# Optimization experiments

Measured on AMD Instinct MI355X. Metric: run time of the kernel, lower is better.

The kernel has to match this reference:

```python
import jax, jax.numpy as jnp
import numpy as np

N = 50000      # nodes
E = 800000     # edges (avg degree 16)
F_IN = 128     # input_dim
HID = 64       # hidden_dim
HEADS = 4      # heads on first layer only
G = 512        # number of graphs in batch
EPS = 1e-5
NEG_SLOPE = 0.2

# (in_dim, out_dim, heads) per GATv2 layer
LAYER_DIMS = [(F_IN, HID, HEADS), (HID * HEADS, HID, 1), (HID, HID, 1)]


def setup_inputs() -> dict:
    key = jax.random.key(0)
    ks = jax.random.split(key, 16)
    def rn(k, shape, fan_in):
        return jax.random.normal(k, shape, jnp.float32) / np.float32(np.sqrt(fan_in))
    inp = {}
    inp["x"] = jax.random.normal(ks[0], (N, F_IN), jnp.float32)
    inp["edge_index"] = jax.random.randint(ks[1], (2, E), 0, N)
    inp["batch"] = jnp.sort(jax.random.randint(ks[2], (N,), 0, G))
    i = 3
    for l, (din, dout, h) in enumerate(LAYER_DIMS):
        kk = jax.random.split(ks[i], 3)
        inp[f"Wl{l}"] = rn(kk[0], (din, h * dout), din)
        inp[f"bl{l}"] = jnp.zeros((h * dout,), jnp.float32)
        inp[f"Wr{l}"] = rn(kk[1], (din, h * dout), din)
        inp[f"br{l}"] = jnp.zeros((h * dout,), jnp.float32)
        inp[f"att{l}"] = rn(kk[2], (h, dout), dout)
        inp[f"bias{l}"] = jnp.zeros((h * dout,), jnp.float32)
        inp[f"ln_g{l}"] = jnp.ones((h * dout,), jnp.float32)
        inp[f"ln_b{l}"] = jnp.zeros((h * dout,), jnp.float32)
        i += 1
    inp["Wh1"] = rn(ks[i], (HID, HID), HID)
    inp["bh1"] = jnp.zeros((HID,), jnp.float32)
    inp["Wh2"] = rn(ks[i + 1], (HID, 1), HID)
    inp["bh2"] = jnp.zeros((1,), jnp.float32)
    return inp


def gatv2_layer(x, src, dst, Wl, bl, Wr, br, att, bias, heads, out_c):
    """PyG GATv2Conv (concat=True, share_weights=False, eval mode)."""
    n = x.shape[0]
    xl = (x @ Wl + bl).reshape(n, heads, out_c)   # messages (source side)
    xr = (x @ Wr + br).reshape(n, heads, out_c)   # destination side
    e = jax.nn.leaky_relu(xl[src] + xr[dst], NEG_SLOPE)          # [E,H,C]
    logit = jnp.einsum('ehc,hc->eh', e, att)                      # [E,H]
    m = jax.ops.segment_max(logit, dst, num_segments=n)           # segment-softmax
    ex = jnp.exp(logit - m[dst])
    den = jax.ops.segment_sum(ex, dst, num_segments=n)
    alpha = ex / den[dst]                                         # [E,H]
    out = jax.ops.segment_sum(alpha[:, :, None] * xl[src], dst, num_segments=n)
    return out.reshape(n, heads * out_c) + bias


def graph_layernorm(h, g, b):
    """PyG LayerNorm(mode='graph') with batch=None: normalize over all elements."""
    mu = h.mean()
    xc = h - mu
    var = (xc * xc).mean()
    return xc * jax.lax.rsqrt(var + EPS) * g + b


def reference(x, edge_index, batch,
              Wl0, bl0, Wr0, br0, att0, bias0, ln_g0, ln_b0,
              Wl1, bl1, Wr1, br1, att1, bias1, ln_g1, ln_b1,
              Wl2, bl2, Wr2, br2, att2, bias2, ln_g2, ln_b2,
              Wh1, bh1, Wh2, bh2):
    src, dst = edge_index[0], edge_index[1]
    layers = [
        (Wl0, bl0, Wr0, br0, att0, bias0, ln_g0, ln_b0),
        (Wl1, bl1, Wr1, br1, att1, bias1, ln_g1, ln_b1),
        (Wl2, bl2, Wr2, br2, att2, bias2, ln_g2, ln_b2),
    ]
    h = x
    for (Wl, bl, Wr, br, att, bias, g, b), (_, dout, heads) in zip(layers, LAYER_DIMS):
        h_in = h
        h = gatv2_layer(h, src, dst, Wl, bl, Wr, br, att, bias, heads, dout)
        h = graph_layernorm(h, g, b)
        h = jax.nn.relu(h)
        if h_in.shape[1] == h.shape[1]:   # residual only when widths match
            h = h + h_in
        # dropout: identity in eval mode
    # global mean pool over graphs
    counts = jax.ops.segment_sum(jnp.ones((h.shape[0], 1), h.dtype), batch, num_segments=G)
    Z = jax.ops.segment_sum(h, batch, num_segments=G) / jnp.maximum(counts, 1.0)
    logits = jax.nn.relu(Z @ Wh1 + bh1) @ Wh2 + bh2
    return logits
```

## Files before the change

### kernel.cpp

```cpp
#include <hip/hip_runtime.h>
#include <math.h>

#define NN 50000
#define NE 800000
#define NG 512
#define LRELU 0.2f
#define LN_EPS 1e-5
#define GCAP 128
#define NBUCK 256

typedef __attribute__((ext_vector_type(8))) short short8;
typedef __attribute__((ext_vector_type(4))) float f32x4;

__global__ void hist_kernel(const int* __restrict__ dst, int* __restrict__ deg) {
    int e = blockIdx.x * blockDim.x + threadIdx.x;
    if (e < NE) atomicAdd(&deg[dst[e]], 1);
}

__global__ __launch_bounds__(1024) void scan1(const int* __restrict__ deg,
                                              int* __restrict__ excl,
                                              int* __restrict__ bsum, int n) {
    __shared__ int s[1024];
    int tid = threadIdx.x;
    int gid = blockIdx.x * 1024 + tid;
    int v = (gid < n) ? deg[gid] : 0;
    s[tid] = v;
    __syncthreads();
    for (int off = 1; off < 1024; off <<= 1) {
        int t = (tid >= off) ? s[tid - off] : 0;
        __syncthreads();
        s[tid] += t;
        __syncthreads();
    }
    if (gid < n) excl[gid] = s[tid] - v;
    if (tid == 1023) bsum[blockIdx.x] = s[1023];
}

__global__ __launch_bounds__(1024) void scan3(int* __restrict__ row_ptr,
                                              int* __restrict__ cursor,
                                              const int* __restrict__ bsum, int n) {
    __shared__ int sbase;
    int tid = threadIdx.x;
    if (tid < 64) {
        int v = (tid < (int)blockIdx.x) ? bsum[tid] : 0;
        #pragma unroll
        for (int off = 32; off > 0; off >>= 1) v += __shfl_xor(v, off, 64);
        if (tid == 0) sbase = v;
    }
    __syncthreads();
    int gid = blockIdx.x * 1024 + tid;
    if (gid < n) {
        int v = row_ptr[gid] + sbase;
        row_ptr[gid] = v;
        cursor[gid] = v;
    }
    if (gid == 0) row_ptr[n] = NE;
}

__global__ void scatter_kernel(const int* __restrict__ src, const int* __restrict__ dst,
                               int* __restrict__ cursor, int* __restrict__ col_src) {
    int e = blockIdx.x * blockDim.x + threadIdx.x;
    if (e < NE) {
        int pos = atomicAdd(&cursor[dst[e]], 1);
        col_src[pos] = src[e];
    }
}

__device__ inline void split_bf16(float v, ushort& h, ushort& l) {
    unsigned ub = __float_as_uint(v);
    unsigned hh = (ub + 0x7FFFu + ((ub >> 16) & 1u)) >> 16;
    float vh = __uint_as_float(hh << 16);
    float r = v - vh;
    unsigned ur = __float_as_uint(r);
    unsigned ll = (ur + 0x7FFFu + ((ur >> 16) & 1u)) >> 16;
    h = (ushort)hh; l = (ushort)ll;
}

__global__ __launch_bounds__(256) void prep_w(const float* __restrict__ Wl0,
                                              const float* __restrict__ Wr0,
                                              const float* __restrict__ Wl1,
                                              const float* __restrict__ Wr1,
                                              const float* __restrict__ Wl2,
                                              const float* __restrict__ Wr2,
                                              ushort* __restrict__ wt) {
    int id = blockIdx.x * 256 + threadIdx.x;
    const float* W; int K, N, rel; ushort* hi;
    if (id < 65536) {
        W = (id < 32768) ? Wl0 : Wr0;
        rel = id & 32767; K = 128; N = 256;
        hi = wt + ((id < 32768) ? 0 : 65536);
    } else if (id < 98304) {
        int t = id - 65536;
        W = (t < 16384) ? Wl1 : Wr1;
        rel = t & 16383; K = 256; N = 64;
        hi = wt + 131072 + ((t < 16384) ? 0 : 32768);
    } else if (id < 106496) {
        int t = id - 98304;
        W = (t < 4096) ? Wl2 : Wr2;
        rel = t & 4095; K = 64; N = 64;
        hi = wt + 196608 + ((t < 4096) ? 0 : 8192);
    } else return;
    ushort* lo = hi + K * N;
    int n = rel / K, k = rel - n * K;
    ushort h, l;
    split_bf16(W[k * N + n], h, l);
    hi[rel] = h;
    lo[rel] = l;
}

template<int NCB, bool DOLN>
__global__ __launch_bounds__(256) void gemm_mfma(const float* __restrict__ A,
                                                 const ushort* __restrict__ Bh0,
                                                 const ushort* __restrict__ Bl0,
                                                 const float* __restrict__ bias0,
                                                 float* __restrict__ C0,
                                                 const ushort* __restrict__ Bh1,
                                                 const ushort* __restrict__ Bl1,
                                                 const float* __restrict__ bias1,
                                                 float* __restrict__ C1,
                                                 int M, int Ncol, int K,
                                                 const double* __restrict__ red,
                                                 int Mdiv,
                                                 const float* __restrict__ lng,
                                                 const float* __restrict__ lnb) {
    __shared__ ushort sAh[64][40];
    __shared__ ushort sAl[64][40];
    __shared__ ushort sBh[64 * NCB][40];
    __shared__ ushort sBl[64 * NCB][40];
    __shared__ float sstat[2];
    const ushort* Bhi = blockIdx.y ? Bh1 : Bh0;
    const ushort* Blo = blockIdx.y ? Bl1 : Bl0;
    const float*  bias = blockIdx.y ? bias1 : bias0;
    float*        C = blockIdx.y ? C1 : C0;
    const int tid = threadIdx.x;
    const int row0 = blockIdx.x * 64;
    const int w = tid >> 6, lane = tid & 63;
    const int fm = lane & 15;
    const int fk = (lane >> 4) * 8;
    float mu = 0.f, rstd = 0.f;
    if constexpr (DOLN) {
        if (tid < 64) {
            double sa = 0, sb = 0;
            for (int i = lane; i < NBUCK; i += 64) { sa += red[2 * i]; sb += red[2 * i + 1]; }
            #pragma unroll
            for (int off = 32; off > 0; off >>= 1) {
                sa += __shfl_xor(sa, off, 64);
                sb += __shfl_xor(sb, off, 64);
            }
            if (lane == 0) {
                double m_ = sa / Mdiv;
                double v_ = sb / Mdiv - m_ * m_;
                sstat[0] = (float)m_;
                sstat[1] = (float)(1.0 / sqrt(v_ + LN_EPS));
            }
        }
        __syncthreads();
        mu = sstat[0]; rstd = sstat[1];
    }
    f32x4 acc[4 * NCB] = {};

    for (int k0 = 0; k0 < K; k0 += 32) {
        __syncthreads();
        int f = tid;
        #pragma unroll
        for (int it = 0; it < 2; it++, f += 256) {
            int r = f >> 3, kc = (f & 7) * 4;
            int grow = row0 + r;
            float4 v = (grow < M) ? *(const float4*)&A[(size_t)grow * K + k0 + kc]
                                  : make_float4(0.f, 0.f, 0.f, 0.f);
            if constexpr (DOLN) {
                int c0 = k0 + kc;
                v.x = fmaxf((v.x - mu) * rstd * lng[c0 + 0] + lnb[c0 + 0], 0.f);
                v.y = fmaxf((v.y - mu) * rstd * lng[c0 + 1] + lnb[c0 + 1], 0.f);
                v.z = fmaxf((v.z - mu) * rstd * lng[c0 + 2] + lnb[c0 + 2], 0.f);
                v.w = fmaxf((v.w - mu) * rstd * lng[c0 + 3] + lnb[c0 + 3], 0.f);
            }
            ushort4 h, l;
            split_bf16(v.x, h.x, l.x);
            split_bf16(v.y, h.y, l.y);
            split_bf16(v.z, h.z, l.z);
            split_bf16(v.w, h.w, l.w);
            *(ushort4*)&sAh[r][kc] = h;
            *(ushort4*)&sAl[r][kc] = l;
        }
        int u = tid;
        #pragma unroll
        for (int it = 0; it < 2 * NCB; it++, u += 256) {
            int n = u >> 3, kc = (u & 7) * 4;
            *(ushort4*)&sBh[n][kc] = *(const ushort4*)&Bhi[(size_t)n * K + k0 + kc];
            *(ushort4*)&sBl[n][kc] = *(const ushort4*)&Blo[(size_t)n * K + k0 + kc];
        }
        __syncthreads();
        short8 ah = *(const short8*)&sAh[w * 16 + fm][fk];
        short8 al = *(const short8*)&sAl[w * 16 + fm][fk];
        #pragma unroll
        for (int c = 0; c < 4 * NCB; c++) {
            short8 bh = *(const short8*)&sBh[c * 16 + fm][fk];
            short8 bl = *(const short8*)&sBl[c * 16 + fm][fk];
            acc[c] = __builtin_amdgcn_mfma_f32_16x16x32_bf16(ah, bh, acc[c], 0, 0, 0);
            acc[c] = __builtin_amdgcn_mfma_f32_16x16x32_bf16(al, bh, acc[c], 0, 0, 0);
            acc[c] = __builtin_amdgcn_mfma_f32_16x16x32_bf16(ah, bl, acc[c], 0, 0, 0);
        }
    }
    const int orow = w * 16 + (lane >> 4) * 4;
    #pragma unroll
    for (int c = 0; c < 4 * NCB; c++) {
        int col = c * 16 + fm;
        float bv = bias[col];
        #pragma unroll
        for (int r = 0; r < 4; r++) {
            int grow = row0 + orow + r;
            if (grow < M) C[(size_t)grow * Ncol + col] = acc[c][r] + bv;
        }
    }
}

__device__ inline float dpp_red_add16(float x) {
    x += __int_as_float(__builtin_amdgcn_update_dpp(0, __float_as_int(x), 0xB1, 0xF, 0xF, true));
    x += __int_as_float(__builtin_amdgcn_update_dpp(0, __float_as_int(x), 0x4E, 0xF, 0xF, true));
    x += __int_as_float(__builtin_amdgcn_update_dpp(0, __float_as_int(x), 0x141, 0xF, 0xF, true));
    x += __int_as_float(__builtin_amdgcn_update_dpp(0, __float_as_int(x), 0x140, 0xF, 0xF, true));
    return x;
}

__device__ inline void gat_upd_fast(const float4& xv, const float4& rxr, const float4& ratt,
                                    float& m, float& sum, float4& acc) {
    float vx = xv.x + rxr.x; vx = fmaxf(vx, vx * LRELU);
    float vy = xv.y + rxr.y; vy = fmaxf(vy, vy * LRELU);
    float vz = xv.z + rxr.z; vz = fmaxf(vz, vz * LRELU);
    float vw = xv.w + rxr.w; vw = fmaxf(vw, vw * LRELU);
    float p = vx * ratt.x;
    p = fmaf(vy, ratt.y, p);
    p = fmaf(vz, ratt.z, p);
    p = fmaf(vw, ratt.w, p);
    p = dpp_red_add16(p);
    if (__all(p <= m)) {
        float e = __expf(p - m);
        sum += e;
        acc.x = fmaf(e, xv.x, acc.x);
        acc.y = fmaf(e, xv.y, acc.y);
        acc.z = fmaf(e, xv.z, acc.z);
        acc.w = fmaf(e, xv.w, acc.w);
    } else {
        float mn = fmaxf(m, p);
        float sc = __expf(m - mn);
        float e  = __expf(p - mn);
        sum = fmaf(sum, sc, e);
        acc.x = fmaf(acc.x, sc, e * xv.x);
        acc.y = fmaf(acc.y, sc, e * xv.y);
        acc.z = fmaf(acc.z, sc, e * xv.z);
        acc.w = fmaf(acc.w, sc, e * xv.w);
        m = mn;
    }
}

__global__ __launch_bounds__(256) void gat4(const float* __restrict__ xl,
                                            const float* __restrict__ xr,
                                            const float* __restrict__ att,
                                            const float* __restrict__ bias,
                                            const int* __restrict__ row_ptr,
                                            const int* __restrict__ col_src,
                                            float* __restrict__ out,
                                            double* __restrict__ red) {
    __shared__ int scol[4][GCAP + 8];
    __shared__ double bs1[4], bs2[4];
    const int tid = threadIdx.x;
    const int w = tid >> 6, lane = tid & 63;
    const int n = blockIdx.x * 4 + w;
    const int base = row_ptr[n];
    int deg = row_ptr[n + 1] - base;
    if (deg > GCAP) deg = GCAP;
    for (int j = lane; j < deg; j += 64) scol[w][j] = col_src[base + j];
    if (deg > 0 && lane < 8) scol[w][deg + lane] = col_src[base + deg - 1];
    const float4 rxr  = ((const float4*)(xr + (size_t)n * 256))[lane];
    const float4 ratt = ((const float4*)att)[lane];
    __syncthreads();

    float m = -1e30f, sum = 0.f;
    float4 acc = {0.f, 0.f, 0.f, 0.f};
    if (deg > 0) {
        auto LD = [&](int j) {
            return ((const float4*)(xl + (size_t)scol[w][j] * 256))[lane];
        };
        float4 b0 = LD(0), b1 = LD(1), b2 = LD(2), b3 = LD(3);
        int j = 0;
        for (; j + 4 <= deg; j += 4) {
            gat_upd_fast(b0, rxr, ratt, m, sum, acc); b0 = LD(j + 4);
            gat_upd_fast(b1, rxr, ratt, m, sum, acc); b1 = LD(j + 5);
            gat_upd_fast(b2, rxr, ratt, m, sum, acc); b2 = LD(j + 6);
            gat_upd_fast(b3, rxr, ratt, m, sum, acc); b3 = LD(j + 7);
        }
        int r = deg - j;
        if (r > 0) gat_upd_fast(b0, rxr, ratt, m, sum, acc);
        if (r > 1) gat_upd_fast(b1, rxr, ratt, m, sum, acc);
        if (r > 2) gat_upd_fast(b2, rxr, ratt, m, sum, acc);
    }
    float rden = (sum > 0.f) ? 1.f / sum : 0.f;
    float4 bv = ((const float4*)bias)[lane];
    float4 o;
    o.x = fmaf(acc.x, rden, bv.x);
    o.y = fmaf(acc.y, rden, bv.y);
    o.z = fmaf(acc.z, rden, bv.z);
    o.w = fmaf(acc.w, rden, bv.w);
    ((float4*)(out + (size_t)n * 256))[lane] = o;

    float z1 = o.x + o.y + o.z + o.w;
    float z2 = o.x * o.x + o.y * o.y + o.z * o.z + o.w * o.w;
    #pragma unroll
    for (int off = 32; off > 0; off >>= 1) {
        z1 += __shfl_xor(z1, off, 64);
        z2 += __shfl_xor(z2, off, 64);
    }
    if (lane == 0) { bs1[w] = (double)z1; bs2[w] = (double)z2; }
    __syncthreads();
    if (tid == 0) {
        double t1 = bs1[0] + bs1[1] + bs1[2] + bs1[3];
        double t2 = bs2[0] + bs2[1] + bs2[2] + bs2[3];
        int b = (blockIdx.x & (NBUCK - 1)) * 2;
        atomicAdd(&red[b], t1);
        atomicAdd(&red[b + 1], t2);
    }
}

__global__ __launch_bounds__(256) void gat1(const float* __restrict__ xl,
                                            const float* __restrict__ xr,
                                            const float* __restrict__ att,
                                            const float* __restrict__ bias,
                                            const int* __restrict__ row_ptr,
                                            const int* __restrict__ col_src,
                                            float* __restrict__ out,
                                            double* __restrict__ red) {
    __shared__ int scol[4][GCAP + 16];
    __shared__ double bs1[4], bs2[4];
    const int tid = threadIdx.x;
    const int w = tid >> 6, lane = tid & 63;
    const int n = blockIdx.x * 4 + w;
    const int g = lane >> 4, li = lane & 15;
    const int base = row_ptr[n];
    int deg = row_ptr[n + 1] - base;
    if (deg > GCAP) deg = GCAP;
    for (int j = lane; j < deg; j += 64) scol[w][j] = col_src[base + j];
    if (deg > 0 && lane < 16) scol[w][deg + lane] = col_src[base + deg - 1];
    const float4 rxr  = ((const float4*)(xr + (size_t)n * 64))[li];
    const float4 ratt = ((const float4*)att)[li];
    __syncthreads();

    float m = -1e30f, sum = 0.f;
    float4 acc = {0.f, 0.f, 0.f, 0.f};
    if (deg > 0) {
        auto LD = [&](int j) {
            return ((const float4*)(xl + (size_t)scol[w][j] * 64))[li];
        };
        float4 a = LD(g), b = LD(g + 4);
        for (int j = g; j < deg; j += 8) {
            gat_upd_fast(a, rxr, ratt, m, sum, acc); a = LD(j + 8);
            if (j + 4 < deg) { gat_upd_fast(b, rxr, ratt, m, sum, acc); b = LD(j + 12); }
        }
    }
    #pragma unroll
    for (int off = 16; off < 64; off <<= 1) {
        float m2 = __shfl_xor(m, off, 64);
        float z2 = __shfl_xor(sum, off, 64);
        float ax = __shfl_xor(acc.x, off, 64);
        float ay = __shfl_xor(acc.y, off, 64);
        float az = __shfl_xor(acc.z, off, 64);
        float aw = __shfl_xor(acc.w, off, 64);
        float M = fmaxf(m, m2);
        float e1 = __expf(m - M), e2 = __expf(m2 - M);
        sum   = sum   * e1 + z2 * e2;
        acc.x = acc.x * e1 + ax * e2;
        acc.y = acc.y * e1 + ay * e2;
        acc.z = acc.z * e1 + az * e2;
        acc.w = acc.w * e1 + aw * e2;
        m = M;
    }
    float rden = (sum > 0.f) ? 1.f / sum : 0.f;
    float4 bv = ((const float4*)bias)[li];
    float4 o;
    o.x = fmaf(acc.x, rden, bv.x);
    o.y = fmaf(acc.y, rden, bv.y);
    o.z = fmaf(acc.z, rden, bv.z);
    o.w = fmaf(acc.w, rden, bv.w);
    if (g == 0) ((float4*)(out + (size_t)n * 64))[li] = o;

    float z1 = (g == 0) ? (o.x + o.y + o.z + o.w) : 0.f;
    float z2 = (g == 0) ? (o.x * o.x + o.y * o.y + o.z * o.z + o.w * o.w) : 0.f;
    #pragma unroll
    for (int off = 32; off > 0; off >>= 1) {
        z1 += __shfl_xor(z1, off, 64);
        z2 += __shfl_xor(z2, off, 64);
    }
    if (lane == 0) { bs1[w] = (double)z1; bs2[w] = (double)z2; }
    __syncthreads();
    if (tid == 0) {
        double t1 = bs1[0] + bs1[1] + bs1[2] + bs1[3];
        double t2 = bs2[0] + bs2[1] + bs2[2] + bs2[3];
        int b = (blockIdx.x & (NBUCK - 1)) * 2;
        atomicAdd(&red[b], t1);
        atomicAdd(&red[b + 1], t2);
    }
}

#define PLB 256
__global__ __launch_bounds__(256) void pool_ln(const float* __restrict__ C2,
                                               const float* __restrict__ D,
                                               const double* __restrict__ red,
                                               const float* __restrict__ g1,
                                               const float* __restrict__ b1,
                                               const float* __restrict__ g2,
                                               const float* __restrict__ b2,
                                               const int* __restrict__ batch,
                                               float* __restrict__ Zsum,
                                               int* __restrict__ gcount) {
    __shared__ float sst[4];
    const int w = threadIdx.x >> 6;
    const int lane = threadIdx.x & 63;
    if (w < 2) {
        const double* rp = red + (w + 1) * 2 * NBUCK;
        double sa = 0, sb = 0;
        for (int i = lane; i < NBUCK; i += 64) { sa += rp[2 * i]; sb += rp[2 * i + 1]; }
        #pragma unroll
        for (int off = 32; off > 0; off >>= 1) {
            sa += __shfl_xor(sa, off, 64);
            sb += __shfl_xor(sb, off, 64);
        }
        if (lane == 0) {
            double m_ = sa / (double)(NN * 64);
            double v_ = sb / (double)(NN * 64) - m_ * m_;
            sst[w * 2]     = (float)m_;
            sst[w * 2 + 1] = (float)(1.0 / sqrt(v_ + LN_EPS));
        }
    }
    __syncthreads();
    const float mu1 = sst[0], r1 = sst[1], mu2 = sst[2], r2 = sst[3];
    const int wid = blockIdx.x * 4 + w;
    const int NW = PLB * 4;
    const int per = (NN + NW - 1) / NW;
    int n0 = wid * per;
    int n1 = n0 + per; if (n1 > NN) n1 = NN;
    if (n0 >= n1) return;
    const float ga = r1 * g1[lane], ba = fmaf(-mu1, ga, b1[lane]);
    const float gb = r2 * g2[lane], bb = fmaf(-mu2, gb, b2[lane]);
    float zacc = 0.f; int cnt = 0; int cur = batch[n0];
    for (int n = n0; n < n1; n++) {
        int gi = batch[n];
        if (gi != cur) {
            atomicAdd(&Zsum[cur * 64 + lane], zacc);
            if (lane == 0) atomicAdd(&gcount[cur], cnt);
            zacc = 0.f; cnt = 0; cur = gi;
        }
        float hin = fmaxf(fmaf(D[(size_t)n * 64 + lane], ga, ba), 0.f);
        float v = fmaxf(fmaf(C2[(size_t)n * 64 + lane], gb, bb), 0.f) + hin;
        zacc += v; cnt++;
    }
    atomicAdd(&Zsum[cur * 64 + lane], zacc);
    if (lane == 0) atomicAdd(&gcount[cur], cnt);
}

__global__ __launch_bounds__(64) void mlp_head(const float* __restrict__ Zsum,
                                               const int* __restrict__ gcount,
                                               const float* __restrict__ Wh1,
                                               const float* __restrict__ bh1,
                                               const float* __restrict__ Wh2,
                                               const float* __restrict__ bh2,
                                               float* __restrict__ out) {
    __shared__ float sz[64];
    int g = blockIdx.x, tid = threadIdx.x;
    int cnt = gcount[g];
    float inv = 1.f / (float)(cnt > 1 ? cnt : 1);
    sz[tid] = Zsum[g * 64 + tid] * inv;
    __syncthreads();
    float acc = bh1[tid];
    #pragma unroll
    for (int c = 0; c < 64; c++) acc = fmaf(sz[c], Wh1[c * 64 + tid], acc);
    acc = fmaxf(acc, 0.f);
    float v = acc * Wh2[tid];
    #pragma unroll
    for (int off = 32; off > 0; off >>= 1) v += __shfl_xor(v, off, 64);
    if (tid == 0) out[g] = v + bh2[0];
}

extern "C" void kernel_launch(void* const* d_in, const int* in_sizes, int n_in,
                              void* d_out, int out_size, void* d_ws, size_t ws_size,
                              hipStream_t stream) {
    (void)in_sizes; (void)n_in; (void)out_size; (void)ws_size;
    const float* x     = (const float*)d_in[0];
    const int*   ei    = (const int*)d_in[1];
    const int*   batch = (const int*)d_in[2];
    const float* Wl0 = (const float*)d_in[3];  const float* bl0 = (const float*)d_in[4];
    const float* Wr0 = (const float*)d_in[5];  const float* br0 = (const float*)d_in[6];
    const float* at0 = (const float*)d_in[7];  const float* bi0 = (const float*)d_in[8];
    const float* lg0 = (const float*)d_in[9];  const float* lb0 = (const float*)d_in[10];
    const float* Wl1 = (const float*)d_in[11]; const float* bl1 = (const float*)d_in[12];
    const float* Wr1 = (const float*)d_in[13]; const float* br1 = (const float*)d_in[14];
    const float* at1 = (const float*)d_in[15]; const float* bi1 = (const float*)d_in[16];
    const float* lg1 = (const float*)d_in[17]; const float* lb1 = (const float*)d_in[18];
    const float* Wl2 = (const float*)d_in[19]; const float* bl2 = (const float*)d_in[20];
    const float* Wr2 = (const float*)d_in[21]; const float* br2 = (const float*)d_in[22];
    const float* at2 = (const float*)d_in[23]; const float* bi2 = (const float*)d_in[24];
    const float* lg2 = (const float*)d_in[25]; const float* lb2 = (const float*)d_in[26];
    const float* Wh1 = (const float*)d_in[27]; const float* bh1 = (const float*)d_in[28];
    const float* Wh2 = (const float*)d_in[29]; const float* bh2 = (const float*)d_in[30];
    float* out = (float*)d_out;

    const int* srcp = ei;
    const int* dstp = ei + NE;

    char* w = (char*)d_ws;
    size_t off = 0;
    auto carve = [&](size_t bytes) -> void* {
        void* p = w + off;
        off += (bytes + 255) & ~(size_t)255;
        return p;
    };
    float* A = (float*)carve((size_t)NN * 256 * 4);
    float* B = (float*)carve((size_t)NN * 256 * 4);
    float* C = (float*)carve((size_t)NN * 256 * 4);
    float* D = (float*)carve((size_t)NN * 64 * 4);
    ushort* wt = (ushort*)carve(212992 * 2);
    const size_t REDB = (size_t)3 * NBUCK * 2 * sizeof(double);
    size_t zbytes = REDB + (size_t)NG * 64 * 4 + NG * 4 + (size_t)NN * 4;
    char* zb = (char*)carve(zbytes);
    double* red   = (double*)zb;
    float*  Zsum  = (float*)(zb + REDB);
    int*    gcnt  = (int*)(zb + REDB + (size_t)NG * 64 * 4);
    int*    deg   = (int*)(zb + REDB + (size_t)NG * 64 * 4 + NG * 4);
    int* row_ptr = (int*)carve((size_t)(NN + 1) * 4);
    int* cursor  = (int*)carve((size_t)NN * 4);
    int* col_src = (int*)carve((size_t)NE * 4);
    int* bsum    = (int*)carve(64 * 4);

    const ushort* W0lh = wt;           const ushort* W0ll = wt + 32768;
    const ushort* W0rh = wt + 65536;   const ushort* W0rl = wt + 98304;
    const ushort* W1lh = wt + 131072;  const ushort* W1ll = wt + 147456;
    const ushort* W1rh = wt + 163840;  const ushort* W1rl = wt + 180224;
    const ushort* W2lh = wt + 196608;  const ushort* W2ll = wt + 200704;
    const ushort* W2rh = wt + 204800;  const ushort* W2rl = wt + 208896;

    hipMemsetAsync(zb, 0, zbytes, stream);
    prep_w<<<416, 256, 0, stream>>>(Wl0, Wr0, Wl1, Wr1, Wl2, Wr2, wt);

    hist_kernel<<<(NE + 255) / 256, 256, 0, stream>>>(dstp, deg);
    const int SB = (NN + 1023) / 1024;
    scan1<<<SB, 1024, 0, stream>>>(deg, row_ptr, bsum, NN);
    scan3<<<SB, 1024, 0, stream>>>(row_ptr, cursor, bsum, NN);
    scatter_kernel<<<(NE + 255) / 256, 256, 0, stream>>>(srcp, dstp, cursor, col_src);

    const int GR = (NN + 63) / 64;
    const int GATB = NN / 4;

    gemm_mfma<4, false><<<dim3(GR, 2), 256, 0, stream>>>(x, W0lh, W0ll, bl0, A,
                                                         W0rh, W0rl, br0, B, NN, 256, 128,
                                                         nullptr, 1, nullptr, nullptr);
    gat4<<<GATB, 256, 0, stream>>>(A, B, at0, bi0, row_ptr, col_src, C, red);

    gemm_mfma<1, true><<<dim3(GR, 2), 256, 0, stream>>>(C, W1lh, W1ll, bl1, A,
                                                        W1rh, W1rl, br1, B, NN, 64, 256,
                                                        red, NN * 256, lg0, lb0);
    gat1<<<GATB, 256, 0, stream>>>(A, B, at1, bi1, row_ptr, col_src, D, red + 2 * NBUCK);

    gemm_mfma<1, true><<<dim3(GR, 2), 256, 0, stream>>>(D, W2lh, W2ll, bl2, A,
                                                        W2rh, W2rl, br2, B, NN, 64, 64,
                                                        red + 2 * NBUCK, NN * 64, lg1, lb1);
    gat1<<<GATB, 256, 0, stream>>>(A, B, at2, bi2, row_ptr, col_src, C, red + 4 * NBUCK);

    pool_ln<<<PLB, 256, 0, stream>>>(C, D, red, lg1, lb1, lg2, lb2,
                                     batch, Zsum, gcnt);
    mlp_head<<<NG, 64, 0, stream>>>(Zsum, gcnt, Wh1, bh1, Wh2, bh2, out);
}
```

Before: 572.5 us.

## Fuse left/right projections into one dual GEMM block and simplify GAT prefetch

For layers 1 and 2, one block now computes both the Wl and Wr projections (128 output columns), so each A tile is loaded and layer-normalised once instead of twice across two grid rows. The GAT kernels replace the padded index buffer and unrolled multi-load prefetch with a clamped two-deep rolling prefetch, which drops the padding writes. The dual GEMM uses more shared memory and registers per block and launches half as many blocks. The shallower prefetch may expose more gather latency in the GAT kernels.

```diff
diff --git a/kernel.cpp b/kernel.cpp
--- a/kernel.cpp
+++ b/kernel.cpp
@@ -108,7 +108,7 @@
     lo[rel] = l;
 }
 
-template<int NCB, bool DOLN>
+template<int NCB, bool DUAL, bool DOLN>
 __global__ __launch_bounds__(256) void gemm_mfma(const float* __restrict__ A,
                                                  const ushort* __restrict__ Bh0,
                                                  const ushort* __restrict__ Bl0,
@@ -128,10 +128,10 @@
     __shared__ ushort sBh[64 * NCB][40];
     __shared__ ushort sBl[64 * NCB][40];
     __shared__ float sstat[2];
-    const ushort* Bhi = blockIdx.y ? Bh1 : Bh0;
-    const ushort* Blo = blockIdx.y ? Bl1 : Bl0;
-    const float*  bias = blockIdx.y ? bias1 : bias0;
-    float*        C = blockIdx.y ? C1 : C0;
+    const ushort* Bhi = (!DUAL && blockIdx.y) ? Bh1 : Bh0;
+    const ushort* Blo = (!DUAL && blockIdx.y) ? Bl1 : Bl0;
+    const float*  biasS = (!DUAL && blockIdx.y) ? bias1 : bias0;
+    float*        CS = (!DUAL && blockIdx.y) ? C1 : C0;
     const int tid = threadIdx.x;
     const int row0 = blockIdx.x * 64;
     const int w = tid >> 6, lane = tid & 63;
@@ -187,8 +187,16 @@
         #pragma unroll
         for (int it = 0; it < 2 * NCB; it++, u += 256) {
             int n = u >> 3, kc = (u & 7) * 4;
-            *(ushort4*)&sBh[n][kc] = *(const ushort4*)&Bhi[(size_t)n * K + k0 + kc];
-            *(ushort4*)&sBl[n][kc] = *(const ushort4*)&Blo[(size_t)n * K + k0 + kc];
+            const ushort* ph; const ushort* pl; int nr;
+            if constexpr (DUAL) {
+                bool s1 = n >= (32 * NCB);
+                ph = s1 ? Bh1 : Bh0; pl = s1 ? Bl1 : Bl0;
+                nr = s1 ? n - 32 * NCB : n;
+            } else {
+                ph = Bhi; pl = Blo; nr = n;
+            }
+            *(ushort4*)&sBh[n][kc] = *(const ushort4*)&ph[(size_t)nr * K + k0 + kc];
+            *(ushort4*)&sBl[n][kc] = *(const ushort4*)&pl[(size_t)nr * K + k0 + kc];
         }
         __syncthreads();
         short8 ah = *(const short8*)&sAh[w * 16 + fm][fk];
@@ -205,12 +213,20 @@
     const int orow = w * 16 + (lane >> 4) * 4;
     #pragma unroll
     for (int c = 0; c < 4 * NCB; c++) {
-        int col = c * 16 + fm;
-        float bv = bias[col];
+        float* Cp; const float* bp; int col;
+        if constexpr (DUAL) {
+            bool s1 = c >= 2 * NCB;
+            Cp = s1 ? C1 : C0; bp = s1 ? bias1 : bias0;
+            col = (s1 ? c - 2 * NCB : c) * 16 + fm;
+        } else {
+            Cp = CS; bp = biasS;
+            col = c * 16 + fm;
+        }
+        float bv = bp[col];
         #pragma unroll
         for (int r = 0; r < 4; r++) {
             int grow = row0 + orow + r;
-            if (grow < M) C[(size_t)grow * Ncol + col] = acc[c][r] + bv;
+            if (grow < M) Cp[(size_t)grow * Ncol + col] = acc[c][r] + bv;
         }
     }
 }
@@ -262,7 +278,7 @@
                                             const int* __restrict__ col_src,
                                             float* __restrict__ out,
                                             double* __restrict__ red) {
-    __shared__ int scol[4][GCAP + 8];
+    __shared__ int scol[4][GCAP];
     __shared__ double bs1[4], bs2[4];
     const int tid = threadIdx.x;
     const int w = tid >> 6, lane = tid & 63;
@@ -271,7 +287,6 @@
     int deg = row_ptr[n + 1] - base;
     if (deg > GCAP) deg = GCAP;
     for (int j = lane; j < deg; j += 64) scol[w][j] = col_src[base + j];
-    if (deg > 0 && lane < 8) scol[w][deg + lane] = col_src[base + deg - 1];
     const float4 rxr  = ((const float4*)(xr + (size_t)n * 256))[lane];
     const float4 ratt = ((const float4*)att)[lane];
     __syncthreads();
@@ -279,21 +294,16 @@
     float m = -1e30f, sum = 0.f;
     float4 acc = {0.f, 0.f, 0.f, 0.f};
     if (deg > 0) {
-        auto LD = [&](int j) {
-            return ((const float4*)(xl + (size_t)scol[w][j] * 256))[lane];
-        };
-        float4 b0 = LD(0), b1 = LD(1), b2 = LD(2), b3 = LD(3);
-        int j = 0;
-        for (; j + 4 <= deg; j += 4) {
-            gat_upd_fast(b0, rxr, ratt, m, sum, acc); b0 = LD(j + 4);
-            gat_upd_fast(b1, rxr, ratt, m, sum, acc); b1 = LD(j + 5);
-            gat_upd_fast(b2, rxr, ratt, m, sum, acc); b2 = LD(j + 6);
-            gat_upd_fast(b3, rxr, ratt, m, sum, acc); b3 = LD(j + 7);
-        }
-        int r = deg - j;
-        if (r > 0) gat_upd_fast(b0, rxr, ratt, m, sum, acc);
-        if (r > 1) gat_upd_fast(b1, rxr, ratt, m, sum, acc);
-        if (r > 2) gat_upd_fast(b2, rxr, ratt, m, sum, acc);
+        const int dm1 = deg - 1;
+        float4 xv0 = ((const float4*)(xl + (size_t)scol[w][0] * 256))[lane];
+        float4 xv1 = ((const float4*)(xl + (size_t)scol[w][(1 < dm1) ? 1 : dm1] * 256))[lane];
+        for (int j = 0; j < deg; j++) {
+            float4 xv = xv0;
+            xv0 = xv1;
+            int idx = (j + 2 < deg) ? j + 2 : dm1;
+            xv1 = ((const float4*)(xl + (size_t)scol[w][idx] * 256))[lane];
+            gat_upd_fast(xv, rxr, ratt, m, sum, acc);
+        }
     }
     float rden = (sum > 0.f) ? 1.f / sum : 0.f;
     float4 bv = ((const float4*)bias)[lane];
@@ -330,7 +340,7 @@
                                             const int* __restrict__ col_src,
                                             float* __restrict__ out,
                                             double* __restrict__ red) {
-    __shared__ int scol[4][GCAP + 16];
+    __shared__ int scol[4][GCAP];
     __shared__ double bs1[4], bs2[4];
     const int tid = threadIdx.x;
     const int w = tid >> 6, lane = tid & 63;
@@ -340,7 +350,6 @@
     int deg = row_ptr[n + 1] - base;
     if (deg > GCAP) deg = GCAP;
     for (int j = lane; j < deg; j += 64) scol[w][j] = col_src[base + j];
-    if (deg > 0 && lane < 16) scol[w][deg + lane] = col_src[base + deg - 1];
     const float4 rxr  = ((const float4*)(xr + (size_t)n * 64))[li];
     const float4 ratt = ((const float4*)att)[li];
     __syncthreads();
@@ -348,13 +357,17 @@
     float m = -1e30f, sum = 0.f;
     float4 acc = {0.f, 0.f, 0.f, 0.f};
     if (deg > 0) {
-        auto LD = [&](int j) {
-            return ((const float4*)(xl + (size_t)scol[w][j] * 64))[li];
+        const int dm1 = deg - 1;
+        auto Lg = [&](int j) {
+            int idx = (j < dm1) ? j : dm1;
+            return ((const float4*)(xl + (size_t)scol[w][idx] * 64))[li];
         };
-        float4 a = LD(g), b = LD(g + 4);
-        for (int j = g; j < deg; j += 8) {
-            gat_upd_fast(a, rxr, ratt, m, sum, acc); a = LD(j + 8);
-            if (j + 4 < deg) { gat_upd_fast(b, rxr, ratt, m, sum, acc); b = LD(j + 12); }
+        float4 xv0 = Lg(g), xv1 = Lg(g + 4);
+        for (int j = g; j < deg; j += 4) {
+            float4 xv = xv0;
+            xv0 = xv1;
+            xv1 = Lg(j + 8);
+            gat_upd_fast(xv, rxr, ratt, m, sum, acc);
         }
     }
     #pragma unroll
@@ -549,19 +562,19 @@
     const int GR = (NN + 63) / 64;
     const int GATB = NN / 4;
 
-    gemm_mfma<4, false><<<dim3(GR, 2), 256, 0, stream>>>(x, W0lh, W0ll, bl0, A,
-                                                         W0rh, W0rl, br0, B, NN, 256, 128,
-                                                         nullptr, 1, nullptr, nullptr);
+    gemm_mfma<4, false, false><<<dim3(GR, 2), 256, 0, stream>>>(
+        x, W0lh, W0ll, bl0, A, W0rh, W0rl, br0, B, NN, 256, 128,
+        nullptr, 1, nullptr, nullptr);
     gat4<<<GATB, 256, 0, stream>>>(A, B, at0, bi0, row_ptr, col_src, C, red);
 
-    gemm_mfma<1, true><<<dim3(GR, 2), 256, 0, stream>>>(C, W1lh, W1ll, bl1, A,
-                                                        W1rh, W1rl, br1, B, NN, 64, 256,
-                                                        red, NN * 256, lg0, lb0);
+    gemm_mfma<2, true, true><<<dim3(GR), 256, 0, stream>>>(
+        C, W1lh, W1ll, bl1, A, W1rh, W1rl, br1, B, NN, 64, 256,
+        red, NN * 256, lg0, lb0);
     gat1<<<GATB, 256, 0, stream>>>(A, B, at1, bi1, row_ptr, col_src, D, red + 2 * NBUCK);
 
-    gemm_mfma<1, true><<<dim3(GR, 2), 256, 0, stream>>>(D, W2lh, W2ll, bl2, A,
-                                                        W2rh, W2rl, br2, B, NN, 64, 64,
-                                                        red + 2 * NBUCK, NN * 64, lg1, lb1);
+    gemm_mfma<2, true, true><<<dim3(GR), 256, 0, stream>>>(
+        D, W2lh, W2ll, bl2, A, W2rh, W2rl, br2, B, NN, 64, 64,
+        red + 2 * NBUCK, NN * 64, lg1, lb1);
     gat1<<<GATB, 256, 0, stream>>>(A, B, at2, bi2, row_ptr, col_src, C, red + 4 * NBUCK);
 
     pool_ln<<<PLB, 256, 0, stream>>>(C, D, red, lg1, lb1, lg2, lb2,
```

Result: faster. 549.1 us (median of 2 runs) (-4.1%).
